# Kernel tuning notes

Hardware: AMD Instinct MI355X
Metric: run time of the kernel (lower is better)

Reference implementation:

```python
import jax, jax.numpy as jnp
import numpy as np

B, S, D = 2, 2048, 1024
H, HD = 16, 64


def setup_inputs() -> dict:
    key = jax.random.key(0)
    ks = jax.random.split(key, 10)
    scale = 1.0 / np.sqrt(D)
    inputs_q = jax.random.normal(ks[0], (B, S, D), dtype=jnp.float32)
    inputs_kv = jax.random.normal(ks[1], (B, S, D), dtype=jnp.float32)
    # causal mask, broadcast over batch: True = attend
    mask = jnp.broadcast_to(jnp.tril(jnp.ones((S, S), dtype=bool)), (B, S, S))
    Wq = jax.random.normal(ks[2], (D, H * HD), dtype=jnp.float32) * scale
    bq = jnp.zeros((H * HD,), dtype=jnp.float32)
    Wk = jax.random.normal(ks[3], (D, H * HD), dtype=jnp.float32) * scale
    bk = jnp.zeros((H * HD,), dtype=jnp.float32)
    Wv = jax.random.normal(ks[4], (D, H * HD), dtype=jnp.float32) * scale
    bv = jnp.zeros((H * HD,), dtype=jnp.float32)
    Wo = jax.random.normal(ks[5], (H * HD, D), dtype=jnp.float32) * scale
    bo = jnp.zeros((D,), dtype=jnp.float32)
    return {"inputs_q": inputs_q, "inputs_kv": inputs_kv, "mask": mask,
            "Wq": Wq, "bq": bq, "Wk": Wk, "bk": bk, "Wv": Wv, "bv": bv,
            "Wo": Wo, "bo": bo}


def reference(inputs_q, inputs_kv, mask, Wq, bq, Wk, bk, Wv, bv, Wo, bo):
    b, s_q, _ = inputs_q.shape
    s_k = inputs_kv.shape[1]
    # projections -> [B, S, H, HD]
    q = (inputs_q @ Wq + bq).reshape(b, s_q, H, HD)
    k = (inputs_kv @ Wk + bk).reshape(b, s_k, H, HD)
    v = (inputs_kv @ Wv + bv).reshape(b, s_k, H, HD)
    q = q / jnp.sqrt(jnp.asarray(HD, dtype=q.dtype))
    # scores: [B, H, Sq, Sk]
    attn = jnp.einsum('bqhd,bkhd->bhqk', q, k)
    m = mask[:, None, :, :]  # [B,1,Sq,Sk] broadcast over heads
    attn = jnp.where(m, attn, jnp.asarray(-1e30, dtype=attn.dtype))
    attn = jax.nn.softmax(attn, axis=-1)
    # dropout_rate = 0.0, deterministic -> identity
    out = jnp.einsum('bhqk,bkhd->bqhd', attn, v).reshape(b, s_q, H * HD)
    return out @ Wo + bo
```

## Files before the change

kernel.cpp:

```cpp
#include <hip/hip_runtime.h>

typedef __attribute__((ext_vector_type(4))) float f32x4;
typedef __attribute__((ext_vector_type(8))) short bf16x8;
typedef unsigned short u16;
typedef unsigned int u32;

#define AS1 __attribute__((address_space(1)))
#define AS3 __attribute__((address_space(3)))

__device__ __forceinline__ float fast_exp2(float x){
  return __builtin_amdgcn_exp2f(x);
}

__device__ __forceinline__ u16 f2bf(float x){
  u32 u = __float_as_uint(x);
  u += 0x7fffu + ((u >> 16) & 1u);
  return (u16)(u >> 16);
}
__device__ __forceinline__ u16 f2bf_fast(float x){
  return (u16)((__float_as_uint(x) + 0x8000u) >> 16);
}

__global__ __launch_bounds__(256) void cvt_qkv(const float* __restrict__ s0,
                                               const float* __restrict__ s1,
                                               u16* __restrict__ d0,
                                               u16* __restrict__ d1, int n4)
{
  int i = blockIdx.x * 256 + threadIdx.x;
  if (i >= n4) return;
  const float* src = blockIdx.y ? s1 : s0;
  u16* dst = blockIdx.y ? d1 : d0;
  float4 v = reinterpret_cast<const float4*>(src)[i];
  ushort4 o;
  o.x = f2bf(v.x); o.y = f2bf(v.y); o.z = f2bf(v.z); o.w = f2bf(v.w);
  reinterpret_cast<ushort4*>(dst)[i] = o;
}

__global__ __launch_bounds__(256) void transpose_cvt4(const float* __restrict__ W0,
                                                      const float* __restrict__ W1,
                                                      const float* __restrict__ W2,
                                                      const float* __restrict__ W3,
                                                      u16* __restrict__ dst)
{
  __shared__ float tile[32][33];
  const int z = blockIdx.z;
  const float* src = z == 0 ? W0 : z == 1 ? W1 : z == 2 ? W2 : W3;
  u16* d = dst + (size_t)z * 1024 * 1024;
  int tx = threadIdx.x & 31, ty = threadIdx.x >> 5;
  int k0 = blockIdx.x * 32, n0 = blockIdx.y * 32;
  for (int r = 0; r < 4; ++r)
    tile[ty + r * 8][tx] = src[(size_t)(k0 + ty + r * 8) * 1024 + n0 + tx];
  __syncthreads();
  for (int r = 0; r < 4; ++r)
    d[(size_t)(n0 + ty + r * 8) * 1024 + k0 + tx] = f2bf(tile[tx][ty + r * 8]);
}

__global__ __launch_bounds__(256) void transpose_bf16_b(const u16* __restrict__ src,
                                                        u16* __restrict__ dst, int R, int C)
{
  __shared__ u16 tile[32][34];
  int bb = blockIdx.z;
  const u16* s = src + (size_t)bb * R * C;
  u16* d = dst + (size_t)bb * C * R;
  int r0 = blockIdx.x * 32, c0 = blockIdx.y * 32;
  int tx = threadIdx.x & 31, ty = threadIdx.x >> 5;
  for (int r = 0; r < 4; ++r)
    tile[ty + r * 8][tx] = s[(size_t)(r0 + ty + r * 8) * C + c0 + tx];
  __syncthreads();
  for (int r = 0; r < 4; ++r)
    d[(size_t)(c0 + ty + r * 8) * R + r0 + tx] = tile[tx][ty + r * 8];
}

__global__ __launch_bounds__(256) void gemm_qkv(const u16* __restrict__ Xq,
                                                const u16* __restrict__ Xkv,
                                                const u16* __restrict__ Wt,
                                                const float* __restrict__ bq,
                                                const float* __restrict__ bk,
                                                const float* __restrict__ bv,
                                                u16* __restrict__ Qb,
                                                u16* __restrict__ Kb,
                                                u16* __restrict__ Vb,
                                                int M, int K)
{
  __shared__ u16 lA[128 * 32];
  __shared__ u16 lB[128 * 32];
  const int tid = threadIdx.x;
  const int l = tid & 63, w = tid >> 6;
  const int wr = w >> 1, wc = w & 1;
  const int bm0 = blockIdx.x * 128, bn0 = blockIdx.y * 128;
  const int seg = bn0 >> 10;
  const int nloc0 = bn0 & 1023;
  const u16* A = seg ? Xkv : Xq;
  const float* bias = seg == 0 ? bq : seg == 1 ? bk : bv;
  u16* C = seg == 0 ? Qb : seg == 1 ? Kb : Vb;
  const float scale = seg == 0 ? 0.125f * 1.44269504089f : 1.0f;
  const int lr = l & 15, lg = (l >> 4) * 8;

  f32x4 acc[4][4];
#pragma unroll
  for (int m = 0; m < 4; ++m)
#pragma unroll
    for (int n = 0; n < 4; ++n) acc[m][n] = (f32x4){0.f, 0.f, 0.f, 0.f};

  for (int k0 = 0; k0 < K; k0 += 32){
#pragma unroll
    for (int c = 0; c < 2; ++c){
      int e = (c * 256 + tid) * 8;
      int row = e >> 5, col = e & 31;
      __builtin_amdgcn_global_load_lds(
          (const AS1 u32*)(A + (size_t)(bm0 + row) * K + k0 + col),
          (AS3 u32*)(&lA[e]), 16, 0, 0);
      __builtin_amdgcn_global_load_lds(
          (const AS1 u32*)(Wt + (size_t)(bn0 + row) * K + k0 + col),
          (AS3 u32*)(&lB[e]), 16, 0, 0);
    }
    __syncthreads();
    bf16x8 aF[4], bF[4];
#pragma unroll
    for (int m = 0; m < 4; ++m)
      aF[m] = *reinterpret_cast<const bf16x8*>(&lA[(wr * 64 + m * 16 + lr) * 32 + lg]);
#pragma unroll
    for (int n = 0; n < 4; ++n)
      bF[n] = *reinterpret_cast<const bf16x8*>(&lB[(wc * 64 + n * 16 + lr) * 32 + lg]);
    __builtin_amdgcn_s_setprio(1);
#pragma unroll
    for (int m = 0; m < 4; ++m)
#pragma unroll
      for (int n = 0; n < 4; ++n)
        acc[m][n] = __builtin_amdgcn_mfma_f32_16x16x32_bf16(aF[m], bF[n], acc[m][n], 0, 0, 0);
    __builtin_amdgcn_s_setprio(0);
    __syncthreads();
  }

  const int r0 = (l >> 4) * 4;
#pragma unroll
  for (int m = 0; m < 4; ++m){
#pragma unroll
    for (int n = 0; n < 4; ++n){
      int col = nloc0 + wc * 64 + n * 16 + lr;
      float bv_ = bias[col];
#pragma unroll
      for (int r = 0; r < 4; ++r){
        int row = bm0 + wr * 64 + m * 16 + r0 + r;
        C[(size_t)row * 1024 + col] = f2bf((acc[m][n][r] + bv_) * scale);
      }
    }
  }
}

__global__ __launch_bounds__(256) void gemm_out(const u16* __restrict__ A,
                                                const u16* __restrict__ Bt,
                                                const float* __restrict__ bias,
                                                float* __restrict__ Cf,
                                                int M, int N, int K)
{
  __shared__ u16 lA[64 * 32];
  __shared__ u16 lB[128 * 32];
  const int tid = threadIdx.x;
  const int l = tid & 63, w = tid >> 6;
  const int wr = w >> 1, wc = w & 1;
  const int bm0 = blockIdx.x * 64, bn0 = blockIdx.y * 128;
  const int lr = l & 15, lg = (l >> 4) * 8;

  f32x4 acc[2][4];
#pragma unroll
  for (int m = 0; m < 2; ++m)
#pragma unroll
    for (int n = 0; n < 4; ++n) acc[m][n] = (f32x4){0.f, 0.f, 0.f, 0.f};

  for (int k0 = 0; k0 < K; k0 += 32){
    {
      int e = tid * 8;
      int row = e >> 5, col = e & 31;
      __builtin_amdgcn_global_load_lds(
          (const AS1 u32*)(A + (size_t)(bm0 + row) * K + k0 + col),
          (AS3 u32*)(&lA[e]), 16, 0, 0);
    }
#pragma unroll
    for (int c = 0; c < 2; ++c){
      int e = (c * 256 + tid) * 8;
      int row = e >> 5, col = e & 31;
      __builtin_amdgcn_global_load_lds(
          (const AS1 u32*)(Bt + (size_t)(bn0 + row) * K + k0 + col),
          (AS3 u32*)(&lB[e]), 16, 0, 0);
    }
    __syncthreads();
    bf16x8 aF[2], bF[4];
#pragma unroll
    for (int m = 0; m < 2; ++m)
      aF[m] = *reinterpret_cast<const bf16x8*>(&lA[(wr * 32 + m * 16 + lr) * 32 + lg]);
#pragma unroll
    for (int n = 0; n < 4; ++n)
      bF[n] = *reinterpret_cast<const bf16x8*>(&lB[(wc * 64 + n * 16 + lr) * 32 + lg]);
    __builtin_amdgcn_s_setprio(1);
#pragma unroll
    for (int m = 0; m < 2; ++m)
#pragma unroll
      for (int n = 0; n < 4; ++n)
        acc[m][n] = __builtin_amdgcn_mfma_f32_16x16x32_bf16(aF[m], bF[n], acc[m][n], 0, 0, 0);
    __builtin_amdgcn_s_setprio(0);
    __syncthreads();
  }

  const int r0 = (l >> 4) * 4;
#pragma unroll
  for (int m = 0; m < 2; ++m)
#pragma unroll
    for (int n = 0; n < 4; ++n){
      int col = bn0 + wc * 64 + n * 16 + lr;
      float bv_ = bias[col];
#pragma unroll
      for (int r = 0; r < 4; ++r){
        int row = bm0 + wr * 32 + m * 16 + r0 + r;
        Cf[(size_t)row * N + col] = acc[m][n][r] + bv_;
      }
    }
}

__global__ __launch_bounds__(256) void attn_fwd(const u16* __restrict__ Qb,
                                                const u16* __restrict__ Kb,
                                                const u16* __restrict__ Vt,
                                                u16* __restrict__ AO, int S)
{
  __shared__ u16 lP[4][32 * 72];
  const int tid = threadIdx.x, l = tid & 63, w = tid >> 6;
  const int j = blockIdx.x;
  const int bh = j & 31;
  const int qt = (j < 256) ? (j >> 5) : (15 - ((j >> 5) & 7));
  const int bb = bh >> 4;
  const size_t baseQK = ((size_t)bb * S) * 1024 + (bh & 15) * 64;
  const size_t baseVt = (size_t)bh * 64 * S;
  const int lr = l & 15, g4 = l >> 4, lg = g4 * 8;
  const int q0 = qt * 128 + w * 32;
  const int ntw = ((q0 + 31) >> 6) + 1;

  bf16x8 qf[2][2];
#pragma unroll
  for (int m = 0; m < 2; ++m)
#pragma unroll
    for (int kc = 0; kc < 2; ++kc)
      qf[m][kc] = *reinterpret_cast<const bf16x8*>(
          Qb + baseQK + (size_t)(q0 + m * 16 + lr) * 1024 + kc * 32 + lg);

  bf16x8 ones;
#pragma unroll
  for (int i = 0; i < 8; ++i) ones[i] = (short)0x3F80;

  f32x4 acc_o[2][4];
  f32x4 acc_l[2];
#pragma unroll
  for (int m = 0; m < 2; ++m){
    acc_l[m] = (f32x4){0.f, 0.f, 0.f, 0.f};
#pragma unroll
    for (int n = 0; n < 4; ++n) acc_o[m][n] = (f32x4){0.f, 0.f, 0.f, 0.f};
  }

  u16* myP = (u16*)lP[w];

  for (int t = 0; t < ntw; ++t){
    const int kv0 = t * 64;

    bf16x8 kf[2][4];
#pragma unroll
    for (int kc = 0; kc < 2; ++kc)
#pragma unroll
      for (int n = 0; n < 4; ++n)
        kf[kc][n] = *reinterpret_cast<const bf16x8*>(
            Kb + baseQK + (size_t)(kv0 + n * 16 + lr) * 1024 + kc * 32 + lg);

    f32x4 sA[2][4];
#pragma unroll
    for (int m = 0; m < 2; ++m)
#pragma unroll
      for (int n = 0; n < 4; ++n) sA[m][n] = (f32x4){0.f, 0.f, 0.f, 0.f};
    __builtin_amdgcn_s_setprio(1);
#pragma unroll
    for (int m = 0; m < 2; ++m)
#pragma unroll
      for (int kc = 0; kc < 2; ++kc)
#pragma unroll
        for (int n = 0; n < 4; ++n)
          sA[m][n] = __builtin_amdgcn_mfma_f32_16x16x32_bf16(qf[m][kc], kf[kc][n], sA[m][n], 0, 0, 0);
    __builtin_amdgcn_s_setprio(0);

    bf16x8 vf[2][4];
#pragma unroll
    for (int kc = 0; kc < 2; ++kc)
#pragma unroll
      for (int n = 0; n < 4; ++n)
        vf[kc][n] = *reinterpret_cast<const bf16x8*>(
            Vt + baseVt + (size_t)(n * 16 + lr) * S + kv0 + kc * 32 + lg);

    if (t == ntw - 1){
#pragma unroll
      for (int m = 0; m < 2; ++m)
#pragma unroll
        for (int n = 0; n < 4; ++n){
          int kvg = kv0 + n * 16 + lr;
#pragma unroll
          for (int r = 0; r < 4; ++r){
            int qg = q0 + m * 16 + g4 * 4 + r;
            float e = fast_exp2(sA[m][n][r]);
            sA[m][n][r] = (kvg <= qg) ? e : 0.f;
          }
        }
    } else {
#pragma unroll
      for (int m = 0; m < 2; ++m)
#pragma unroll
        for (int n = 0; n < 4; ++n)
#pragma unroll
          for (int r = 0; r < 4; ++r)
            sA[m][n][r] = fast_exp2(sA[m][n][r]);
    }

#pragma unroll
    for (int m = 0; m < 2; ++m)
#pragma unroll
      for (int n = 0; n < 4; ++n)
#pragma unroll
        for (int r = 0; r < 4; ++r){
          int row = m * 16 + g4 * 4 + r;
          myP[row * 72 + n * 16 + lr] = f2bf_fast(sA[m][n][r]);
        }
    asm volatile("s_waitcnt lgkmcnt(0)" ::: "memory");
    __builtin_amdgcn_sched_barrier(0);

    bf16x8 pf[2][2];
#pragma unroll
    for (int m = 0; m < 2; ++m)
#pragma unroll
      for (int kc = 0; kc < 2; ++kc)
        pf[m][kc] = *reinterpret_cast<const bf16x8*>(&myP[(m * 16 + lr) * 72 + (kc * 4 + g4) * 8]);

    __builtin_amdgcn_s_setprio(1);
#pragma unroll
    for (int m = 0; m < 2; ++m)
#pragma unroll
      for (int kc = 0; kc < 2; ++kc){
        acc_l[m] = __builtin_amdgcn_mfma_f32_16x16x32_bf16(pf[m][kc], ones, acc_l[m], 0, 0, 0);
#pragma unroll
        for (int n = 0; n < 4; ++n)
          acc_o[m][n] = __builtin_amdgcn_mfma_f32_16x16x32_bf16(pf[m][kc], vf[kc][n], acc_o[m][n], 0, 0, 0);
      }
    __builtin_amdgcn_s_setprio(0);
  }

#pragma unroll
  for (int m = 0; m < 2; ++m){
    float inv[4];
#pragma unroll
    for (int r = 0; r < 4; ++r) inv[r] = 1.0f / acc_l[m][r];
#pragma unroll
    for (int n = 0; n < 4; ++n)
#pragma unroll
      for (int r = 0; r < 4; ++r){
        int row = q0 + m * 16 + g4 * 4 + r;
        AO[baseQK + (size_t)row * 1024 + n * 16 + lr] = f2bf(acc_o[m][n][r] * inv[r]);
      }
  }
}

extern "C" void kernel_launch(void* const* d_in, const int* in_sizes, int n_in,
                              void* d_out, int out_size, void* d_ws, size_t ws_size,
                              hipStream_t stream)
{
  const float* inq  = (const float*)d_in[0];
  const float* inkv = (const float*)d_in[1];
  const float* Wq = (const float*)d_in[3];
  const float* bq = (const float*)d_in[4];
  const float* Wk = (const float*)d_in[5];
  const float* bk = (const float*)d_in[6];
  const float* Wv = (const float*)d_in[7];
  const float* bv = (const float*)d_in[8];
  const float* Wo = (const float*)d_in[9];
  const float* bo = (const float*)d_in[10];
  float* out = (float*)d_out;

  const int B = 2, S = 2048, D = 1024;
  const int M = B * S;

  char* ws = (char*)d_ws;
  const size_t MB = 1024ull * 1024ull;
  u16* Xq  = (u16*)(ws + 0 * MB);
  u16* Vtg = (u16*)(ws + 0 * MB);
  u16* Xkv = (u16*)(ws + 8 * MB);
  u16* Wt  = (u16*)(ws + 16 * MB);
  u16* Wot = (u16*)(ws + 22 * MB);
  u16* Qb  = (u16*)(ws + 24 * MB);
  u16* Kb  = (u16*)(ws + 32 * MB);
  u16* Vb  = (u16*)(ws + 40 * MB);
  u16* AOb = (u16*)(ws + 48 * MB);

  cvt_qkv<<<dim3(M * D / 4 / 256, 2), 256, 0, stream>>>(inq, inkv, Xq, Xkv, M * D / 4);

  transpose_cvt4<<<dim3(32, 32, 4), 256, 0, stream>>>(Wq, Wk, Wv, Wo, Wt);

  gemm_qkv<<<dim3(M / 128, 3072 / 128), 256, 0, stream>>>(Xq, Xkv, Wt, bq, bk, bv,
                                                          Qb, Kb, Vb, M, D);

  transpose_bf16_b<<<dim3(S / 32, D / 32, B), 256, 0, stream>>>(Vb, Vtg, S, D);

  attn_fwd<<<dim3(512), 256, 0, stream>>>(Qb, Kb, Vtg, AOb, S);

  gemm_out<<<dim3(M / 64, D / 128), 256, 0, stream>>>(AOb, Wot, bo, out, M, D, D);
}
```

Before: 141.8 us.

## Double-buffer K tile loads in attention loop with register ping-pong

Restructures the attention inner loop into a two-stage software pipeline. The next K tile is prefetched into an alternate register buffer, and V is loaded before the QK MFMAs, so global load latency overlaps with compute. It also sets a minimum of 2 blocks per CU in launch bounds and removes the explicit LDS waitcnt/sched barrier. The extra buffers raise VGPR pressure and may cause spills under the occupancy constraint.

```diff
diff --git a/kernel.cpp b/kernel.cpp
--- a/kernel.cpp
+++ b/kernel.cpp
@@ -217,10 +217,79 @@
     }
 }
 
-__global__ __launch_bounds__(256) void attn_fwd(const u16* __restrict__ Qb,
-                                                const u16* __restrict__ Kb,
-                                                const u16* __restrict__ Vt,
-                                                u16* __restrict__ AO, int S)
+
+#define LOADK(KF, T) do{                                                      \
+  const int kv0_ = (T) * 64;                                                  \
+  _Pragma("unroll") for (int kc_ = 0; kc_ < 2; ++kc_)                         \
+  _Pragma("unroll") for (int n_ = 0; n_ < 4; ++n_)                            \
+    KF[kc_][n_] = *reinterpret_cast<const bf16x8*>(                           \
+        Kb + baseQK + (size_t)(kv0_ + n_ * 16 + lr) * 1024 + kc_ * 32 + lg);  \
+}while(0)
+
+#define LOADV(VF, T) do{                                                      \
+  const int kv0_ = (T) * 64;                                                  \
+  _Pragma("unroll") for (int kc_ = 0; kc_ < 2; ++kc_)                         \
+  _Pragma("unroll") for (int n_ = 0; n_ < 4; ++n_)                            \
+    VF[kc_][n_] = *reinterpret_cast<const bf16x8*>(                           \
+        Vt + baseVt + (size_t)(n_ * 16 + lr) * S + kv0_ + kc_ * 32 + lg);     \
+}while(0)
+
+#define ATTN_BODY(KF, VF, T) do{                                              \
+  const int kv0_ = (T) * 64;                                                  \
+  f32x4 sA_[2][4];                                                            \
+  _Pragma("unroll") for (int m_ = 0; m_ < 2; ++m_)                            \
+  _Pragma("unroll") for (int n_ = 0; n_ < 4; ++n_)                            \
+    sA_[m_][n_] = (f32x4){0.f, 0.f, 0.f, 0.f};                                \
+  __builtin_amdgcn_s_setprio(1);                                              \
+  _Pragma("unroll") for (int m_ = 0; m_ < 2; ++m_)                            \
+  _Pragma("unroll") for (int kc_ = 0; kc_ < 2; ++kc_)                         \
+  _Pragma("unroll") for (int n_ = 0; n_ < 4; ++n_)                            \
+    sA_[m_][n_] = __builtin_amdgcn_mfma_f32_16x16x32_bf16(                    \
+        qf[m_][kc_], KF[kc_][n_], sA_[m_][n_], 0, 0, 0);                      \
+  __builtin_amdgcn_s_setprio(0);                                              \
+  if ((T) == ntw - 1){                                                        \
+    _Pragma("unroll") for (int m_ = 0; m_ < 2; ++m_)                          \
+    _Pragma("unroll") for (int n_ = 0; n_ < 4; ++n_){                         \
+      int kvg_ = kv0_ + n_ * 16 + lr;                                         \
+      _Pragma("unroll") for (int r_ = 0; r_ < 4; ++r_){                       \
+        int qg_ = q0 + m_ * 16 + g4 * 4 + r_;                                 \
+        float e_ = fast_exp2(sA_[m_][n_][r_]);                                \
+        sA_[m_][n_][r_] = (kvg_ <= qg_) ? e_ : 0.f;                           \
+      }                                                                       \
+    }                                                                         \
+  } else {                                                                    \
+    _Pragma("unroll") for (int m_ = 0; m_ < 2; ++m_)                          \
+    _Pragma("unroll") for (int n_ = 0; n_ < 4; ++n_)                          \
+    _Pragma("unroll") for (int r_ = 0; r_ < 4; ++r_)                          \
+      sA_[m_][n_][r_] = fast_exp2(sA_[m_][n_][r_]);                           \
+  }                                                                           \
+  _Pragma("unroll") for (int m_ = 0; m_ < 2; ++m_)                            \
+  _Pragma("unroll") for (int n_ = 0; n_ < 4; ++n_)                            \
+  _Pragma("unroll") for (int r_ = 0; r_ < 4; ++r_){                           \
+    int row_ = m_ * 16 + g4 * 4 + r_;                                         \
+    myP[row_ * 72 + n_ * 16 + lr] = f2bf_fast(sA_[m_][n_][r_]);               \
+  }                                                                           \
+  bf16x8 pf_[2][2];                                                           \
+  _Pragma("unroll") for (int m_ = 0; m_ < 2; ++m_)                            \
+  _Pragma("unroll") for (int kc_ = 0; kc_ < 2; ++kc_)                         \
+    pf_[m_][kc_] = *reinterpret_cast<const bf16x8*>(                          \
+        &myP[(m_ * 16 + lr) * 72 + (kc_ * 4 + g4) * 8]);                      \
+  __builtin_amdgcn_s_setprio(1);                                              \
+  _Pragma("unroll") for (int m_ = 0; m_ < 2; ++m_)                            \
+  _Pragma("unroll") for (int kc_ = 0; kc_ < 2; ++kc_){                        \
+    acc_l[m_] = __builtin_amdgcn_mfma_f32_16x16x32_bf16(                      \
+        pf_[m_][kc_], ones, acc_l[m_], 0, 0, 0);                              \
+    _Pragma("unroll") for (int n_ = 0; n_ < 4; ++n_)                          \
+      acc_o[m_][n_] = __builtin_amdgcn_mfma_f32_16x16x32_bf16(                \
+          pf_[m_][kc_], VF[kc_][n_], acc_o[m_][n_], 0, 0, 0);                 \
+  }                                                                           \
+  __builtin_amdgcn_s_setprio(0);                                              \
+}while(0)
+
+__global__ __launch_bounds__(256, 2) void attn_fwd(const u16* __restrict__ Qb,
+                                                   const u16* __restrict__ Kb,
+                                                   const u16* __restrict__ Vt,
+                                                   u16* __restrict__ AO, int S)
 {
   __shared__ u16 lP[4][32 * 72];
   const int tid = threadIdx.x, l = tid & 63, w = tid >> 6;
@@ -257,93 +326,24 @@
 
   u16* myP = (u16*)lP[w];
 
-  for (int t = 0; t < ntw; ++t){
-    const int kv0 = t * 64;
-
-    bf16x8 kf[2][4];
-#pragma unroll
-    for (int kc = 0; kc < 2; ++kc)
-#pragma unroll
-      for (int n = 0; n < 4; ++n)
-        kf[kc][n] = *reinterpret_cast<const bf16x8*>(
-            Kb + baseQK + (size_t)(kv0 + n * 16 + lr) * 1024 + kc * 32 + lg);
-
-    f32x4 sA[2][4];
-#pragma unroll
-    for (int m = 0; m < 2; ++m)
-#pragma unroll
-      for (int n = 0; n < 4; ++n) sA[m][n] = (f32x4){0.f, 0.f, 0.f, 0.f};
-    __builtin_amdgcn_s_setprio(1);
-#pragma unroll
-    for (int m = 0; m < 2; ++m)
-#pragma unroll
-      for (int kc = 0; kc < 2; ++kc)
-#pragma unroll
-        for (int n = 0; n < 4; ++n)
-          sA[m][n] = __builtin_amdgcn_mfma_f32_16x16x32_bf16(qf[m][kc], kf[kc][n], sA[m][n], 0, 0, 0);
-    __builtin_amdgcn_s_setprio(0);
-
-    bf16x8 vf[2][4];
-#pragma unroll
-    for (int kc = 0; kc < 2; ++kc)
-#pragma unroll
-      for (int n = 0; n < 4; ++n)
-        vf[kc][n] = *reinterpret_cast<const bf16x8*>(
-            Vt + baseVt + (size_t)(n * 16 + lr) * S + kv0 + kc * 32 + lg);
-
-    if (t == ntw - 1){
-#pragma unroll
-      for (int m = 0; m < 2; ++m)
-#pragma unroll
-        for (int n = 0; n < 4; ++n){
-          int kvg = kv0 + n * 16 + lr;
-#pragma unroll
-          for (int r = 0; r < 4; ++r){
-            int qg = q0 + m * 16 + g4 * 4 + r;
-            float e = fast_exp2(sA[m][n][r]);
-            sA[m][n][r] = (kvg <= qg) ? e : 0.f;
-          }
-        }
-    } else {
-#pragma unroll
-      for (int m = 0; m < 2; ++m)
-#pragma unroll
-        for (int n = 0; n < 4; ++n)
-#pragma unroll
-          for (int r = 0; r < 4; ++r)
-            sA[m][n][r] = fast_exp2(sA[m][n][r]);
-    }
-
-#pragma unroll
-    for (int m = 0; m < 2; ++m)
-#pragma unroll
-      for (int n = 0; n < 4; ++n)
-#pragma unroll
-        for (int r = 0; r < 4; ++r){
-          int row = m * 16 + g4 * 4 + r;
-          myP[row * 72 + n * 16 + lr] = f2bf_fast(sA[m][n][r]);
-        }
-    asm volatile("s_waitcnt lgkmcnt(0)" ::: "memory");
-    __builtin_amdgcn_sched_barrier(0);
-
-    bf16x8 pf[2][2];
-#pragma unroll
-    for (int m = 0; m < 2; ++m)
-#pragma unroll
-      for (int kc = 0; kc < 2; ++kc)
-        pf[m][kc] = *reinterpret_cast<const bf16x8*>(&myP[(m * 16 + lr) * 72 + (kc * 4 + g4) * 8]);
-
-    __builtin_amdgcn_s_setprio(1);
-#pragma unroll
-    for (int m = 0; m < 2; ++m)
-#pragma unroll
-      for (int kc = 0; kc < 2; ++kc){
-        acc_l[m] = __builtin_amdgcn_mfma_f32_16x16x32_bf16(pf[m][kc], ones, acc_l[m], 0, 0, 0);
-#pragma unroll
-        for (int n = 0; n < 4; ++n)
-          acc_o[m][n] = __builtin_amdgcn_mfma_f32_16x16x32_bf16(pf[m][kc], vf[kc][n], acc_o[m][n], 0, 0, 0);
-      }
-    __builtin_amdgcn_s_setprio(0);
+  bf16x8 kfA[2][4], kfB[2][4];
+  LOADK(kfA, 0);
+  int t = 0;
+  while (true){
+    {
+      bf16x8 vf_[2][4];
+      LOADV(vf_, t);
+      if (t + 1 < ntw) LOADK(kfB, t + 1);
+      ATTN_BODY(kfA, vf_, t);
+    }
+    ++t; if (t == ntw) break;
+    {
+      bf16x8 vf_[2][4];
+      LOADV(vf_, t);
+      if (t + 1 < ntw) LOADK(kfA, t + 1);
+      ATTN_BODY(kfB, vf_, t);
+    }
+    ++t; if (t == ntw) break;
   }
 
 #pragma unroll
```

Result: no change. 142.0 us (+0.1%).

## Fuse V transpose into QKV GEMM and stage K/V through swizzled LDS

Applied to the files above, without the earlier changes.

The QKV GEMM epilogue now writes V straight into a tiled, transposed per-head layout, so the separate transpose kernel and its launch go away. The attention kernel moves to 32-wide KV tiles. Each wave prefetches the next K and V tiles into private swizzled LDS buffers with async global-to-LDS loads, overlapping memory with compute. Query tiles are assigned as complementary causal pairs across waves to balance work, and launch bounds ask for 2 blocks per CU. The cost is more LDS traffic, smaller MFMA batches per iteration, and more waitcnt synchronisation.

```diff
diff --git a/kernel.cpp b/kernel.cpp
--- a/kernel.cpp
+++ b/kernel.cpp
@@ -7,6 +7,11 @@
 
 #define AS1 __attribute__((address_space(1)))
 #define AS3 __attribute__((address_space(3)))
+
+#define WAITVM(N) do{ asm volatile("s_waitcnt vmcnt(" #N ")" ::: "memory"); \
+                      __builtin_amdgcn_sched_barrier(0); }while(0)
+#define LGKM0     do{ asm volatile("s_waitcnt lgkmcnt(0)" ::: "memory");    \
+                      __builtin_amdgcn_sched_barrier(0); }while(0)
 
 __device__ __forceinline__ float fast_exp2(float x){
   return __builtin_amdgcn_exp2f(x);
@@ -55,22 +60,6 @@
     d[(size_t)(n0 + ty + r * 8) * 1024 + k0 + tx] = f2bf(tile[tx][ty + r * 8]);
 }
 
-__global__ __launch_bounds__(256) void transpose_bf16_b(const u16* __restrict__ src,
-                                                        u16* __restrict__ dst, int R, int C)
-{
-  __shared__ u16 tile[32][34];
-  int bb = blockIdx.z;
-  const u16* s = src + (size_t)bb * R * C;
-  u16* d = dst + (size_t)bb * C * R;
-  int r0 = blockIdx.x * 32, c0 = blockIdx.y * 32;
-  int tx = threadIdx.x & 31, ty = threadIdx.x >> 5;
-  for (int r = 0; r < 4; ++r)
-    tile[ty + r * 8][tx] = s[(size_t)(r0 + ty + r * 8) * C + c0 + tx];
-  __syncthreads();
-  for (int r = 0; r < 4; ++r)
-    d[(size_t)(c0 + ty + r * 8) * R + r0 + tx] = tile[tx][ty + r * 8];
-}
-
 __global__ __launch_bounds__(256) void gemm_qkv(const u16* __restrict__ Xq,
                                                 const u16* __restrict__ Xkv,
                                                 const u16* __restrict__ Wt,
@@ -79,7 +68,7 @@
                                                 const float* __restrict__ bv,
                                                 u16* __restrict__ Qb,
                                                 u16* __restrict__ Kb,
-                                                u16* __restrict__ Vb,
+                                                u16* __restrict__ Vtb,
                                                 int M, int K)
 {
   __shared__ u16 lA[128 * 32];
@@ -92,7 +81,6 @@
   const int nloc0 = bn0 & 1023;
   const u16* A = seg ? Xkv : Xq;
   const float* bias = seg == 0 ? bq : seg == 1 ? bk : bv;
-  u16* C = seg == 0 ? Qb : seg == 1 ? Kb : Vb;
   const float scale = seg == 0 ? 0.125f * 1.44269504089f : 1.0f;
   const int lr = l & 15, lg = (l >> 4) * 8;
 
@@ -133,18 +121,37 @@
   }
 
   const int r0 = (l >> 4) * 4;
-#pragma unroll
-  for (int m = 0; m < 4; ++m){
-#pragma unroll
-    for (int n = 0; n < 4; ++n){
-      int col = nloc0 + wc * 64 + n * 16 + lr;
-      float bv_ = bias[col];
-#pragma unroll
-      for (int r = 0; r < 4; ++r){
-        int row = bm0 + wr * 64 + m * 16 + r0 + r;
-        C[(size_t)row * 1024 + col] = f2bf((acc[m][n][r] + bv_) * scale);
+  if (seg < 2){
+    u16* C = seg == 0 ? Qb : Kb;
+#pragma unroll
+    for (int m = 0; m < 4; ++m)
+#pragma unroll
+      for (int n = 0; n < 4; ++n){
+        int col = nloc0 + wc * 64 + n * 16 + lr;
+        float bv_ = bias[col];
+#pragma unroll
+        for (int r = 0; r < 4; ++r){
+          int row = bm0 + wr * 64 + m * 16 + r0 + r;
+          C[(size_t)row * 1024 + col] = f2bf((acc[m][n][r] + bv_) * scale);
+        }
       }
-    }
+  } else {
+#pragma unroll
+    for (int m = 0; m < 4; ++m)
+#pragma unroll
+      for (int n = 0; n < 4; ++n){
+        int col = nloc0 + wc * 64 + n * 16 + lr;
+        float bv_ = bias[col];
+        int h = col >> 6, hdl = col & 63;
+#pragma unroll
+        for (int r = 0; r < 4; ++r){
+          int row = bm0 + wr * 64 + m * 16 + r0 + r;
+          int b = row >> 11, kv = row & 2047;
+          size_t off = ((size_t)(b * 16 + h)) * 131072 +
+                       (size_t)(kv >> 5) * 2048 + hdl * 32 + (kv & 31);
+          Vtb[off] = f2bf(acc[m][n][r] + bv_);
+        }
+      }
   }
 }
 
@@ -217,22 +224,37 @@
     }
 }
 
-__global__ __launch_bounds__(256) void attn_fwd(const u16* __restrict__ Qb,
-                                                const u16* __restrict__ Kb,
-                                                const u16* __restrict__ Vt,
-                                                u16* __restrict__ AO, int S)
-{
-  __shared__ u16 lP[4][32 * 72];
+
+__global__ __launch_bounds__(256, 2) void attn_fwd(const u16* __restrict__ Qb,
+                                                   const u16* __restrict__ Kb,
+                                                   const u16* __restrict__ Vtb,
+                                                   u16* __restrict__ AO, int S)
+{
+  __shared__ u16 lK[4][32 * 64];
+  __shared__ u16 lV[4][64 * 32];
+  __shared__ u16 lP[4][32 * 36];
   const int tid = threadIdx.x, l = tid & 63, w = tid >> 6;
   const int j = blockIdx.x;
-  const int bh = j & 31;
-  const int qt = (j < 256) ? (j >> 5) : (15 - ((j >> 5) & 7));
+  const int half = j >> 8;
+  const int jj = j & 255;
+  const int bh = jj >> 3;
+  const int k = half * 8 + (jj & 7);
+  const int i1 = 2 * k, i2 = 2 * k + 1;
+  int c;
+  if (!half) c = (w == 0) ? i1 : (w == 1) ? 63 - i1 : (w == 2) ? i2 : 63 - i2;
+  else       c = (w == 0) ? 63 - i1 : (w == 1) ? i1 : (w == 2) ? 63 - i2 : i2;
+
   const int bb = bh >> 4;
   const size_t baseQK = ((size_t)bb * S) * 1024 + (bh & 15) * 64;
-  const size_t baseVt = (size_t)bh * 64 * S;
+  const u16* gK = Kb + baseQK;
+  const u16* gV = Vtb + (size_t)bh * 131072;
   const int lr = l & 15, g4 = l >> 4, lg = g4 * 8;
-  const int q0 = qt * 128 + w * 32;
-  const int ntw = ((q0 + 31) >> 6) + 1;
+  const int q0 = c * 32;
+  const int ntw = c + 1;
+
+  u16* lKw = (u16*)lK[w];
+  u16* lVw = (u16*)lV[w];
+  u16* lPw = (u16*)lP[w];
 
   bf16x8 qf[2][2];
 #pragma unroll
@@ -255,94 +277,111 @@
     for (int n = 0; n < 4; ++n) acc_o[m][n] = (f32x4){0.f, 0.f, 0.f, 0.f};
   }
 
-  u16* myP = (u16*)lP[w];
+  WAITVM(0);
+
+#define STAGE_K(T) do{                                                        \
+  const size_t rb_ = (size_t)(T) * 32 * 1024;                                 \
+  _Pragma("unroll") for (int i_ = 0; i_ < 4; ++i_){                           \
+    int s_ = i_ * 64 + l; int row_ = s_ >> 3, ch_ = s_ & 7;                   \
+    __builtin_amdgcn_global_load_lds(                                         \
+        (const AS1 u32*)(gK + rb_ + (size_t)row_ * 1024 + ((ch_ ^ (row_ & 7)) * 8)), \
+        (AS3 u32*)(lKw + i_ * 512), 16, 0, 0);                                \
+  }                                                                           \
+}while(0)
+#define STAGE_V(T) do{                                                        \
+  const size_t rb_ = (size_t)(T) * 2048;                                      \
+  _Pragma("unroll") for (int i_ = 0; i_ < 4; ++i_){                           \
+    int s_ = i_ * 64 + l; int row_ = s_ >> 2, ch_ = s_ & 3;                   \
+    __builtin_amdgcn_global_load_lds(                                         \
+        (const AS1 u32*)(gV + rb_ + row_ * 32 + ((ch_ ^ (row_ & 3)) * 8)),    \
+        (AS3 u32*)(lVw + i_ * 512), 16, 0, 0);                                \
+  }                                                                           \
+}while(0)
+
+  STAGE_K(0);
+  STAGE_V(0);
 
   for (int t = 0; t < ntw; ++t){
-    const int kv0 = t * 64;
-
-    bf16x8 kf[2][4];
-#pragma unroll
-    for (int kc = 0; kc < 2; ++kc)
-#pragma unroll
-      for (int n = 0; n < 4; ++n)
-        kf[kc][n] = *reinterpret_cast<const bf16x8*>(
-            Kb + baseQK + (size_t)(kv0 + n * 16 + lr) * 1024 + kc * 32 + lg);
-
-    f32x4 sA[2][4];
+    const int kv0 = t * 32;
+    const int tn = (t + 1 < ntw) ? t + 1 : t;
+
+    WAITVM(4);
+    bf16x8 kfr[2][2];
+#pragma unroll
+    for (int np = 0; np < 2; ++np)
+#pragma unroll
+      for (int kc = 0; kc < 2; ++kc){
+        int row = np * 16 + lr, ch = kc * 4 + g4;
+        kfr[np][kc] = *reinterpret_cast<const bf16x8*>(
+            reinterpret_cast<const char*>(lKw) + row * 128 + ((ch ^ (row & 7)) << 4));
+      }
+    LGKM0;
+    STAGE_K(tn);
+
+    f32x4 sA[2][2];
 #pragma unroll
     for (int m = 0; m < 2; ++m)
 #pragma unroll
-      for (int n = 0; n < 4; ++n) sA[m][n] = (f32x4){0.f, 0.f, 0.f, 0.f};
+      for (int np = 0; np < 2; ++np) sA[m][np] = (f32x4){0.f, 0.f, 0.f, 0.f};
     __builtin_amdgcn_s_setprio(1);
 #pragma unroll
     for (int m = 0; m < 2; ++m)
 #pragma unroll
       for (int kc = 0; kc < 2; ++kc)
 #pragma unroll
-        for (int n = 0; n < 4; ++n)
-          sA[m][n] = __builtin_amdgcn_mfma_f32_16x16x32_bf16(qf[m][kc], kf[kc][n], sA[m][n], 0, 0, 0);
+        for (int np = 0; np < 2; ++np)
+          sA[m][np] = __builtin_amdgcn_mfma_f32_16x16x32_bf16(qf[m][kc], kfr[np][kc], sA[m][np], 0, 0, 0);
     __builtin_amdgcn_s_setprio(0);
 
-    bf16x8 vf[2][4];
-#pragma unroll
-    for (int kc = 0; kc < 2; ++kc)
-#pragma unroll
-      for (int n = 0; n < 4; ++n)
-        vf[kc][n] = *reinterpret_cast<const bf16x8*>(
-            Vt + baseVt + (size_t)(n * 16 + lr) * S + kv0 + kc * 32 + lg);
-
     if (t == ntw - 1){
 #pragma unroll
       for (int m = 0; m < 2; ++m)
 #pragma unroll
-        for (int n = 0; n < 4; ++n){
-          int kvg = kv0 + n * 16 + lr;
+        for (int np = 0; np < 2; ++np){
+          int kvg = kv0 + np * 16 + lr;
 #pragma unroll
           for (int r = 0; r < 4; ++r){
             int qg = q0 + m * 16 + g4 * 4 + r;
-            float e = fast_exp2(sA[m][n][r]);
-            sA[m][n][r] = (kvg <= qg) ? e : 0.f;
+            float e = fast_exp2(sA[m][np][r]);
+            float p = (kvg <= qg) ? e : 0.f;
+            lPw[(m * 16 + g4 * 4 + r) * 36 + np * 16 + lr] = f2bf_fast(p);
           }
         }
     } else {
 #pragma unroll
       for (int m = 0; m < 2; ++m)
 #pragma unroll
-        for (int n = 0; n < 4; ++n)
+        for (int np = 0; np < 2; ++np)
 #pragma unroll
           for (int r = 0; r < 4; ++r)
-            sA[m][n][r] = fast_exp2(sA[m][n][r]);
-    }
-
+            lPw[(m * 16 + g4 * 4 + r) * 36 + np * 16 + lr] =
+                f2bf_fast(fast_exp2(sA[m][np][r]));
+    }
+
+    WAITVM(4);
+    bf16x8 vfr[4];
+#pragma unroll
+    for (int n = 0; n < 4; ++n){
+      int row = n * 16 + lr;
+      vfr[n] = *reinterpret_cast<const bf16x8*>(
+          reinterpret_cast<const char*>(lVw) + row * 64 + ((g4 ^ (row & 3)) << 4));
+    }
+    bf16x8 pf[2];
 #pragma unroll
     for (int m = 0; m < 2; ++m)
+      pf[m] = *reinterpret_cast<const bf16x8*>(
+          reinterpret_cast<const char*>(lPw) + (m * 16 + lr) * 72 + g4 * 16);
+    LGKM0;
+    STAGE_V(tn);
+
+    __builtin_amdgcn_s_setprio(1);
+#pragma unroll
+    for (int m = 0; m < 2; ++m){
+      acc_l[m] = __builtin_amdgcn_mfma_f32_16x16x32_bf16(pf[m], ones, acc_l[m], 0, 0, 0);
 #pragma unroll
       for (int n = 0; n < 4; ++n)
-#pragma unroll
-        for (int r = 0; r < 4; ++r){
-          int row = m * 16 + g4 * 4 + r;
-          myP[row * 72 + n * 16 + lr] = f2bf_fast(sA[m][n][r]);
-        }
-    asm volatile("s_waitcnt lgkmcnt(0)" ::: "memory");
-    __builtin_amdgcn_sched_barrier(0);
-
-    bf16x8 pf[2][2];
-#pragma unroll
-    for (int m = 0; m < 2; ++m)
-#pragma unroll
-      for (int kc = 0; kc < 2; ++kc)
-        pf[m][kc] = *reinterpret_cast<const bf16x8*>(&myP[(m * 16 + lr) * 72 + (kc * 4 + g4) * 8]);
-
-    __builtin_amdgcn_s_setprio(1);
-#pragma unroll
-    for (int m = 0; m < 2; ++m)
-#pragma unroll
-      for (int kc = 0; kc < 2; ++kc){
-        acc_l[m] = __builtin_amdgcn_mfma_f32_16x16x32_bf16(pf[m][kc], ones, acc_l[m], 0, 0, 0);
-#pragma unroll
-        for (int n = 0; n < 4; ++n)
-          acc_o[m][n] = __builtin_amdgcn_mfma_f32_16x16x32_bf16(pf[m][kc], vf[kc][n], acc_o[m][n], 0, 0, 0);
-      }
+        acc_o[m][n] = __builtin_amdgcn_mfma_f32_16x16x32_bf16(pf[m], vfr[n], acc_o[m][n], 0, 0, 0);
+    }
     __builtin_amdgcn_s_setprio(0);
   }
 
@@ -359,6 +398,8 @@
         AO[baseQK + (size_t)row * 1024 + n * 16 + lr] = f2bf(acc_o[m][n][r] * inv[r]);
       }
   }
+#undef STAGE_K
+#undef STAGE_V
 }
 
 extern "C" void kernel_launch(void* const* d_in, const int* in_sizes, int n_in,
@@ -383,13 +424,12 @@
   char* ws = (char*)d_ws;
   const size_t MB = 1024ull * 1024ull;
   u16* Xq  = (u16*)(ws + 0 * MB);
-  u16* Vtg = (u16*)(ws + 0 * MB);
   u16* Xkv = (u16*)(ws + 8 * MB);
   u16* Wt  = (u16*)(ws + 16 * MB);
   u16* Wot = (u16*)(ws + 22 * MB);
   u16* Qb  = (u16*)(ws + 24 * MB);
   u16* Kb  = (u16*)(ws + 32 * MB);
-  u16* Vb  = (u16*)(ws + 40 * MB);
+  u16* Vtb = (u16*)(ws + 40 * MB);
   u16* AOb = (u16*)(ws + 48 * MB);
 
   cvt_qkv<<<dim3(M * D / 4 / 256, 2), 256, 0, stream>>>(inq, inkv, Xq, Xkv, M * D / 4);
@@ -397,11 +437,9 @@
   transpose_cvt4<<<dim3(32, 32, 4), 256, 0, stream>>>(Wq, Wk, Wv, Wo, Wt);
 
   gemm_qkv<<<dim3(M / 128, 3072 / 128), 256, 0, stream>>>(Xq, Xkv, Wt, bq, bk, bv,
-                                                          Qb, Kb, Vb, M, D);
-
-  transpose_bf16_b<<<dim3(S / 32, D / 32, B), 256, 0, stream>>>(Vb, Vtg, S, D);
-
-  attn_fwd<<<dim3(512), 256, 0, stream>>>(Qb, Kb, Vtg, AOb, S);
+                                                          Qb, Kb, Vtb, M, D);
+
+  attn_fwd<<<dim3(512), 256, 0, stream>>>(Qb, Kb, Vtb, AOb, S);
 
   gemm_out<<<dim3(M / 64, D / 128), 256, 0, stream>>>(AOb, Wot, bo, out, M, D, D);
 }
```

After: 152.8 us. 7.7% more time.

## Stage K/V tiles in LDS shared by 8 waves and fuse V transpose into QKV GEMM

Applied to the files above, without the earlier changes.

The attention kernel now uses 512-thread blocks where eight waves of 16 query rows each share swizzled K and V tiles loaded into LDS by global_load_lds. Previously each wave read K/V directly from global memory. Each block processes a paired short and long causal query tile to balance work, with XCD-aware head mapping. The V projection epilogue writes the transposed layout directly, which removes the separate transpose kernel. The cost is two block-wide barriers per KV tile and strided scattered 2-byte stores in the V epilogue.

```diff
diff --git a/kernel.cpp b/kernel.cpp
--- a/kernel.cpp
+++ b/kernel.cpp
@@ -55,22 +55,6 @@
     d[(size_t)(n0 + ty + r * 8) * 1024 + k0 + tx] = f2bf(tile[tx][ty + r * 8]);
 }
 
-__global__ __launch_bounds__(256) void transpose_bf16_b(const u16* __restrict__ src,
-                                                        u16* __restrict__ dst, int R, int C)
-{
-  __shared__ u16 tile[32][34];
-  int bb = blockIdx.z;
-  const u16* s = src + (size_t)bb * R * C;
-  u16* d = dst + (size_t)bb * C * R;
-  int r0 = blockIdx.x * 32, c0 = blockIdx.y * 32;
-  int tx = threadIdx.x & 31, ty = threadIdx.x >> 5;
-  for (int r = 0; r < 4; ++r)
-    tile[ty + r * 8][tx] = s[(size_t)(r0 + ty + r * 8) * C + c0 + tx];
-  __syncthreads();
-  for (int r = 0; r < 4; ++r)
-    d[(size_t)(c0 + ty + r * 8) * R + r0 + tx] = tile[tx][ty + r * 8];
-}
-
 __global__ __launch_bounds__(256) void gemm_qkv(const u16* __restrict__ Xq,
                                                 const u16* __restrict__ Xkv,
                                                 const u16* __restrict__ Wt,
@@ -79,7 +63,7 @@
                                                 const float* __restrict__ bv,
                                                 u16* __restrict__ Qb,
                                                 u16* __restrict__ Kb,
-                                                u16* __restrict__ Vb,
+                                                u16* __restrict__ Vt,
                                                 int M, int K)
 {
   __shared__ u16 lA[128 * 32];
@@ -92,7 +76,6 @@
   const int nloc0 = bn0 & 1023;
   const u16* A = seg ? Xkv : Xq;
   const float* bias = seg == 0 ? bq : seg == 1 ? bk : bv;
-  u16* C = seg == 0 ? Qb : seg == 1 ? Kb : Vb;
   const float scale = seg == 0 ? 0.125f * 1.44269504089f : 1.0f;
   const int lr = l & 15, lg = (l >> 4) * 8;
 
@@ -133,18 +116,36 @@
   }
 
   const int r0 = (l >> 4) * 4;
-#pragma unroll
-  for (int m = 0; m < 4; ++m){
-#pragma unroll
-    for (int n = 0; n < 4; ++n){
-      int col = nloc0 + wc * 64 + n * 16 + lr;
-      float bv_ = bias[col];
-#pragma unroll
-      for (int r = 0; r < 4; ++r){
-        int row = bm0 + wr * 64 + m * 16 + r0 + r;
-        C[(size_t)row * 1024 + col] = f2bf((acc[m][n][r] + bv_) * scale);
-      }
-    }
+  if (seg < 2){
+    u16* C = seg == 0 ? Qb : Kb;
+#pragma unroll
+    for (int m = 0; m < 4; ++m)
+#pragma unroll
+      for (int n = 0; n < 4; ++n){
+        int col = nloc0 + wc * 64 + n * 16 + lr;
+        float bv_ = bias[col];
+#pragma unroll
+        for (int r = 0; r < 4; ++r){
+          int row = bm0 + wr * 64 + m * 16 + r0 + r;
+          C[(size_t)row * 1024 + col] = f2bf((acc[m][n][r] + bv_) * scale);
+        }
+      }
+  } else {
+#pragma unroll
+    for (int m = 0; m < 4; ++m)
+#pragma unroll
+      for (int n = 0; n < 4; ++n){
+        int col = nloc0 + wc * 64 + n * 16 + lr;
+        float bv_ = bias[col];
+        int h = col >> 6, hdl = col & 63;
+#pragma unroll
+        for (int r = 0; r < 4; ++r){
+          int row = bm0 + wr * 64 + m * 16 + r0 + r;
+          int b = row >> 11, kv = row & 2047;
+          size_t off = ((size_t)(b * 16 + h)) * 131072 + (size_t)hdl * 2048 + kv;
+          Vt[off] = f2bf(acc[m][n][r] + bv_);
+        }
+      }
   }
 }
 
@@ -217,148 +218,132 @@
     }
 }
 
-__global__ __launch_bounds__(256) void attn_fwd(const u16* __restrict__ Qb,
-                                                const u16* __restrict__ Kb,
-                                                const u16* __restrict__ Vt,
-                                                u16* __restrict__ AO, int S)
-{
-  __shared__ u16 lP[4][32 * 72];
+
+__global__ __launch_bounds__(512, 2) void attn_fwd(const u16* __restrict__ Qb,
+                                                   const u16* __restrict__ Kb,
+                                                   const u16* __restrict__ Vt,
+                                                   u16* __restrict__ AO, int S)
+{
+  __shared__ u16 lK[64 * 64];
+  __shared__ u16 lV[64 * 64];
+  __shared__ u16 lP[8][16 * 72];
   const int tid = threadIdx.x, l = tid & 63, w = tid >> 6;
   const int j = blockIdx.x;
-  const int bh = j & 31;
-  const int qt = (j < 256) ? (j >> 5) : (15 - ((j >> 5) & 7));
+  const int xcd = j & 7;
+  const int bh = xcd * 4 + ((j >> 3) & 3);
+  const int p = j >> 5;
   const int bb = bh >> 4;
   const size_t baseQK = ((size_t)bb * S) * 1024 + (bh & 15) * 64;
-  const size_t baseVt = (size_t)bh * 64 * S;
+  const u16* gK = Kb + baseQK;
+  const u16* gV = Vt + (size_t)bh * 131072;
   const int lr = l & 15, g4 = l >> 4, lg = g4 * 8;
-  const int q0 = qt * 128 + w * 32;
-  const int ntw = ((q0 + 31) >> 6) + 1;
-
-  bf16x8 qf[2][2];
-#pragma unroll
-  for (int m = 0; m < 2; ++m)
+
+  u16* lPw = (u16*)lP[w];
+  bf16x8 ones;
+#pragma unroll
+  for (int i = 0; i < 8; ++i) ones[i] = (short)0x3F80;
+
+#define STAGE_KV(T) do{                                                       \
+  int row_ = tid >> 3, ch_ = tid & 7, sc_ = (ch_ ^ (row_ & 7)) * 8;           \
+  __builtin_amdgcn_global_load_lds(                                           \
+      (const AS1 u32*)(gK + (size_t)(64 * (T) + row_) * 1024 + sc_),          \
+      (AS3 u32*)(lK + tid * 8), 16, 0, 0);                                    \
+  __builtin_amdgcn_global_load_lds(                                           \
+      (const AS1 u32*)(gV + (size_t)row_ * 2048 + 64 * (T) + sc_),            \
+      (AS3 u32*)(lV + tid * 8), 16, 0, 0);                                    \
+}while(0)
+
+#pragma unroll
+  for (int pass = 0; pass < 2; ++pass){
+    const int qt = pass ? (15 - p) : p;
+    const int ntb = 2 * qt + 2;
+    const int q0 = qt * 128 + w * 16;
+
+    bf16x8 qf[2];
 #pragma unroll
     for (int kc = 0; kc < 2; ++kc)
-      qf[m][kc] = *reinterpret_cast<const bf16x8*>(
-          Qb + baseQK + (size_t)(q0 + m * 16 + lr) * 1024 + kc * 32 + lg);
-
-  bf16x8 ones;
-#pragma unroll
-  for (int i = 0; i < 8; ++i) ones[i] = (short)0x3F80;
-
-  f32x4 acc_o[2][4];
-  f32x4 acc_l[2];
-#pragma unroll
-  for (int m = 0; m < 2; ++m){
-    acc_l[m] = (f32x4){0.f, 0.f, 0.f, 0.f};
-#pragma unroll
-    for (int n = 0; n < 4; ++n) acc_o[m][n] = (f32x4){0.f, 0.f, 0.f, 0.f};
-  }
-
-  u16* myP = (u16*)lP[w];
-
-  for (int t = 0; t < ntw; ++t){
-    const int kv0 = t * 64;
-
-    bf16x8 kf[2][4];
-#pragma unroll
-    for (int kc = 0; kc < 2; ++kc)
-#pragma unroll
-      for (int n = 0; n < 4; ++n)
-        kf[kc][n] = *reinterpret_cast<const bf16x8*>(
-            Kb + baseQK + (size_t)(kv0 + n * 16 + lr) * 1024 + kc * 32 + lg);
-
-    f32x4 sA[2][4];
-#pragma unroll
-    for (int m = 0; m < 2; ++m)
-#pragma unroll
-      for (int n = 0; n < 4; ++n) sA[m][n] = (f32x4){0.f, 0.f, 0.f, 0.f};
-    __builtin_amdgcn_s_setprio(1);
-#pragma unroll
-    for (int m = 0; m < 2; ++m)
-#pragma unroll
-      for (int kc = 0; kc < 2; ++kc)
-#pragma unroll
-        for (int n = 0; n < 4; ++n)
-          sA[m][n] = __builtin_amdgcn_mfma_f32_16x16x32_bf16(qf[m][kc], kf[kc][n], sA[m][n], 0, 0, 0);
-    __builtin_amdgcn_s_setprio(0);
-
-    bf16x8 vf[2][4];
-#pragma unroll
-    for (int kc = 0; kc < 2; ++kc)
-#pragma unroll
-      for (int n = 0; n < 4; ++n)
-        vf[kc][n] = *reinterpret_cast<const bf16x8*>(
-            Vt + baseVt + (size_t)(n * 16 + lr) * S + kv0 + kc * 32 + lg);
-
-    if (t == ntw - 1){
-#pragma unroll
-      for (int m = 0; m < 2; ++m)
-#pragma unroll
-        for (int n = 0; n < 4; ++n){
-          int kvg = kv0 + n * 16 + lr;
-#pragma unroll
-          for (int r = 0; r < 4; ++r){
-            int qg = q0 + m * 16 + g4 * 4 + r;
-            float e = fast_exp2(sA[m][n][r]);
-            sA[m][n][r] = (kvg <= qg) ? e : 0.f;
+      qf[kc] = *reinterpret_cast<const bf16x8*>(
+          Qb + baseQK + (size_t)(q0 + lr) * 1024 + kc * 32 + lg);
+
+    f32x4 acc_o[4], acc_l;
+    acc_l = (f32x4){0.f, 0.f, 0.f, 0.f};
+#pragma unroll
+    for (int n = 0; n < 4; ++n) acc_o[n] = (f32x4){0.f, 0.f, 0.f, 0.f};
+
+    for (int t = 0; t < ntb; ++t){
+      STAGE_KV(t);
+      __syncthreads();
+
+      if (64 * t <= q0 + 15){
+        f32x4 sA[4];
+#pragma unroll
+        for (int np = 0; np < 4; ++np) sA[np] = (f32x4){0.f, 0.f, 0.f, 0.f};
+        __builtin_amdgcn_s_setprio(1);
+#pragma unroll
+        for (int kc = 0; kc < 2; ++kc)
+#pragma unroll
+          for (int np = 0; np < 4; ++np){
+            int row = np * 16 + lr, ch = kc * 4 + g4;
+            bf16x8 kf = *reinterpret_cast<const bf16x8*>(
+                reinterpret_cast<const char*>(lK) + row * 128 + ((ch ^ (row & 7)) << 4));
+            sA[np] = __builtin_amdgcn_mfma_f32_16x16x32_bf16(qf[kc], kf, sA[np], 0, 0, 0);
+          }
+        __builtin_amdgcn_s_setprio(0);
+
+        const bool needmask = (64 * t + 63 > q0);
+        if (needmask){
+#pragma unroll
+          for (int np = 0; np < 4; ++np){
+            int kvg = 64 * t + np * 16 + lr;
+#pragma unroll
+            for (int r = 0; r < 4; ++r){
+              int qg = q0 + g4 * 4 + r;
+              float e = fast_exp2(sA[np][r]);
+              lPw[(g4 * 4 + r) * 72 + np * 16 + lr] = f2bf_fast((kvg <= qg) ? e : 0.f);
+            }
+          }
+        } else {
+#pragma unroll
+          for (int np = 0; np < 4; ++np)
+#pragma unroll
+            for (int r = 0; r < 4; ++r)
+              lPw[(g4 * 4 + r) * 72 + np * 16 + lr] = f2bf_fast(fast_exp2(sA[np][r]));
+        }
+
+        bf16x8 pf[2];
+#pragma unroll
+        for (int kc = 0; kc < 2; ++kc)
+          pf[kc] = *reinterpret_cast<const bf16x8*>(
+              reinterpret_cast<const char*>(lPw) + lr * 144 + (kc * 4 + g4) * 16);
+        __builtin_amdgcn_s_setprio(1);
+#pragma unroll
+        for (int kc = 0; kc < 2; ++kc){
+          acc_l = __builtin_amdgcn_mfma_f32_16x16x32_bf16(pf[kc], ones, acc_l, 0, 0, 0);
+#pragma unroll
+          for (int n = 0; n < 4; ++n){
+            int row = n * 16 + lr, ch = kc * 4 + g4;
+            bf16x8 vf = *reinterpret_cast<const bf16x8*>(
+                reinterpret_cast<const char*>(lV) + row * 128 + ((ch ^ (row & 7)) << 4));
+            acc_o[n] = __builtin_amdgcn_mfma_f32_16x16x32_bf16(pf[kc], vf, acc_o[n], 0, 0, 0);
           }
         }
-    } else {
-#pragma unroll
-      for (int m = 0; m < 2; ++m)
-#pragma unroll
-        for (int n = 0; n < 4; ++n)
-#pragma unroll
-          for (int r = 0; r < 4; ++r)
-            sA[m][n][r] = fast_exp2(sA[m][n][r]);
-    }
-
-#pragma unroll
-    for (int m = 0; m < 2; ++m)
-#pragma unroll
-      for (int n = 0; n < 4; ++n)
-#pragma unroll
-        for (int r = 0; r < 4; ++r){
-          int row = m * 16 + g4 * 4 + r;
-          myP[row * 72 + n * 16 + lr] = f2bf_fast(sA[m][n][r]);
-        }
-    asm volatile("s_waitcnt lgkmcnt(0)" ::: "memory");
-    __builtin_amdgcn_sched_barrier(0);
-
-    bf16x8 pf[2][2];
-#pragma unroll
-    for (int m = 0; m < 2; ++m)
-#pragma unroll
-      for (int kc = 0; kc < 2; ++kc)
-        pf[m][kc] = *reinterpret_cast<const bf16x8*>(&myP[(m * 16 + lr) * 72 + (kc * 4 + g4) * 8]);
-
-    __builtin_amdgcn_s_setprio(1);
-#pragma unroll
-    for (int m = 0; m < 2; ++m)
-#pragma unroll
-      for (int kc = 0; kc < 2; ++kc){
-        acc_l[m] = __builtin_amdgcn_mfma_f32_16x16x32_bf16(pf[m][kc], ones, acc_l[m], 0, 0, 0);
-#pragma unroll
-        for (int n = 0; n < 4; ++n)
-          acc_o[m][n] = __builtin_amdgcn_mfma_f32_16x16x32_bf16(pf[m][kc], vf[kc][n], acc_o[m][n], 0, 0, 0);
-      }
-    __builtin_amdgcn_s_setprio(0);
+        __builtin_amdgcn_s_setprio(0);
+      }
+      __syncthreads();
+    }
+
+    float inv[4];
+#pragma unroll
+    for (int r = 0; r < 4; ++r) inv[r] = 1.0f / acc_l[r];
+#pragma unroll
+    for (int n = 0; n < 4; ++n)
+#pragma unroll
+      for (int r = 0; r < 4; ++r){
+        int row = q0 + g4 * 4 + r;
+        AO[baseQK + (size_t)row * 1024 + n * 16 + lr] = f2bf(acc_o[n][r] * inv[r]);
+      }
   }
-
-#pragma unroll
-  for (int m = 0; m < 2; ++m){
-    float inv[4];
-#pragma unroll
-    for (int r = 0; r < 4; ++r) inv[r] = 1.0f / acc_l[m][r];
-#pragma unroll
-    for (int n = 0; n < 4; ++n)
-#pragma unroll
-      for (int r = 0; r < 4; ++r){
-        int row = q0 + m * 16 + g4 * 4 + r;
-        AO[baseQK + (size_t)row * 1024 + n * 16 + lr] = f2bf(acc_o[m][n][r] * inv[r]);
-      }
-  }
+#undef STAGE_KV
 }
 
 extern "C" void kernel_launch(void* const* d_in, const int* in_sizes, int n_in,
@@ -383,13 +368,12 @@
   char* ws = (char*)d_ws;
   const size_t MB = 1024ull * 1024ull;
   u16* Xq  = (u16*)(ws + 0 * MB);
-  u16* Vtg = (u16*)(ws + 0 * MB);
   u16* Xkv = (u16*)(ws + 8 * MB);
   u16* Wt  = (u16*)(ws + 16 * MB);
   u16* Wot = (u16*)(ws + 22 * MB);
   u16* Qb  = (u16*)(ws + 24 * MB);
   u16* Kb  = (u16*)(ws + 32 * MB);
-  u16* Vb  = (u16*)(ws + 40 * MB);
+  u16* Vtg = (u16*)(ws + 40 * MB);
   u16* AOb = (u16*)(ws + 48 * MB);
 
   cvt_qkv<<<dim3(M * D / 4 / 256, 2), 256, 0, stream>>>(inq, inkv, Xq, Xkv, M * D / 4);
@@ -397,11 +381,9 @@
   transpose_cvt4<<<dim3(32, 32, 4), 256, 0, stream>>>(Wq, Wk, Wv, Wo, Wt);
 
   gemm_qkv<<<dim3(M / 128, 3072 / 128), 256, 0, stream>>>(Xq, Xkv, Wt, bq, bk, bv,
-                                                          Qb, Kb, Vb, M, D);
-
-  transpose_bf16_b<<<dim3(S / 32, D / 32, B), 256, 0, stream>>>(Vb, Vtg, S, D);
-
-  attn_fwd<<<dim3(512), 256, 0, stream>>>(Qb, Kb, Vtg, AOb, S);
+                                                          Qb, Kb, Vtg, M, D);
+
+  attn_fwd<<<dim3(256), 512, 0, stream>>>(Qb, Kb, Vtg, AOb, S);
 
   gemm_out<<<dim3(M / 64, D / 128), 256, 0, stream>>>(AOb, Wot, bo, out, M, D, D);
 }
```

After: 134.0 us. 5.5% less time.
